# Performance work log

Hardware: AMD Instinct MI355X
Metric: run time of the kernel (lower is better)

## Reference

```python
import jax, jax.numpy as jnp
import numpy as np

GMAX = 1.0   # args.gmax
GMIN = 0.01  # args.gmin
EPS = 0.1    # args.e_train


def setup_inputs() -> dict:
    key = jax.random.key(0)
    k1, k2, k3, k4 = jax.random.split(key, 4)
    N, B, NIN, NOUT, E = 8, 32, 128, 128, 1024
    # analog signals live in [0, 1]
    a_previous = jax.random.uniform(k1, (N, B, NIN, E), dtype=jnp.float32)
    # conductance params (clamped to [-gmax, gmax] in forward)
    theta = jax.random.uniform(k2, (NIN + 2, NOUT), dtype=jnp.float32) * 2.0 - 1.0
    # per-replica multiplicative noise seed in [0, 1); forward maps to 1 +- eps
    noise = jax.random.uniform(k3, (N, NIN + 2, NOUT), dtype=jnp.float32)
    # printed-tanh activation params eta = [offset, scale, shift, slope]
    eta = jnp.array([0.0, 1.0, 0.0, 1.0], dtype=jnp.float32) + 0.1 * jax.random.normal(k4, (4,), dtype=jnp.float32)
    return {"a_previous": a_previous, "theta": theta, "noise": noise, "eta": eta}


def reference(a_previous, theta, noise, eta):
    sg = jax.lax.stop_gradient
    # theta property: clamp + gmin pruning with straight-through estimator
    t = jnp.clip(theta, -GMAX, GMAX)
    t = jnp.where(jnp.abs(t) < GMIN, 0.0, t)
    theta_eff = sg(t) + theta - sg(theta)
    # theta_noisy: replicate over N with multiplicative uniform noise in [1-eps, 1+eps]
    theta_noisy = theta_eff[None, :, :] * ((noise * 2.0 - 1.0) * EPS + 1.0)  # [N, M, O], M = n_in+2
    # W: abs-normalized conductances per output column group
    abs_tn = jnp.abs(theta_noisy)
    W = abs_tn / (jnp.sum(abs_tn, axis=1, keepdims=True) + 1e-10)
    # sign masks (constants w.r.t. grad: values fully overwritten in torch)
    pos = sg((theta_noisy >= 0.0).astype(theta_noisy.dtype))
    neg = 1.0 - pos
    # a: [N, B, n_in, E] -> [N, B, E, n_in]; append ones and zeros columns
    a_r = jnp.transpose(a_previous, (0, 1, 3, 2))
    ones = jnp.ones(a_r.shape[:3] + (1,), a_r.dtype)
    zeros = jnp.zeros_like(ones)
    a_ext = jnp.concatenate([a_r, ones, zeros], axis=3)  # [N, B, E, M]
    # INV: unipolar complement; zero the last (zeros) column after inversion
    a_neg = (1.0 - a_ext).at[..., -1].set(0.0)
    # split-sign MAC: z [N, B, E, n_out]
    z = (jnp.einsum('nbem,nmo->nbeo', a_ext, W * pos)
         + jnp.einsum('nbem,nmo->nbeo', a_neg, W * neg))
    # printed tanh activation
    act = eta[0] + eta[1] * jnp.tanh((z - eta[2]) * eta[3])
    # back to [N, B, n_out, E]
    return jnp.transpose(act, (0, 1, 3, 2))
```

## Files before the change

kernel.cpp:

```cpp
#include <hip/hip_runtime.h>
#include <hip/hip_bf16.h>
#include <stdint.h>

#define N_REP 8
#define BATCH 32
#define NIN   128
#define NOUT  128
#define EDIM  1024
#define MDIM  130
#define ETILE 64
#define NGRP  32
#define GSTR  260

typedef __attribute__((ext_vector_type(8))) short short8;
typedef __attribute__((ext_vector_type(4))) float f32x4;

__device__ __forceinline__ unsigned short f2bf(float f) {
    union { float f; uint32_t u; } v;
    v.f = f;
    uint32_t u = v.u;
    uint32_t r = u + 0x7fffu + ((u >> 16) & 1u);
    return (unsigned short)(r >> 16);
}

__device__ __forceinline__ uint32_t pk2bf(float lo, float hi) {
    __hip_bfloat162 h = __float22bfloat162_rn(make_float2(lo, hi));
    uint32_t d;
    __builtin_memcpy(&d, &h, 4);
    return d;
}

__device__ __forceinline__ void gload_lds16(float* lds, const float* g) {
    __builtin_amdgcn_global_load_lds(
        (const __attribute__((address_space(1))) void*)g,
        (__attribute__((address_space(3))) void*)lds, 16, 0, 0);
}

__global__ __launch_bounds__(64)
void prep_kernel(const float* __restrict__ theta,
                 const float* __restrict__ noise,
                 unsigned short* __restrict__ Sg,
                 float* __restrict__ biasg) {
    const int n = blockIdx.x >> 7;
    const int o = blockIdx.x & 127;
    const int lane = threadIdx.x;

    const float* nb = noise + (size_t)n * MDIM * NOUT + o;
    auto tn_at = [&](int m) -> float {
        float t = theta[m * NOUT + o];
        t = fminf(fmaxf(t, -1.f), 1.f);
        if (fabsf(t) < 0.01f) t = 0.f;
        return t * fmaf(nb[m * NOUT], 0.2f, 0.9f);
    };

    const float t0 = tn_at(lane);
    const float t1 = tn_at(lane + 64);
    const float t2 = (lane < 2) ? tn_at(128 + lane) : 0.f;

    float s = fabsf(t0) + fabsf(t1) + fabsf(t2);
#pragma unroll
    for (int d = 1; d < 64; d <<= 1) s += __shfl_xor(s, d, 64);
    const float inv = 1.f / (s + 1e-10f);

    const float w0 = fabsf(t0) * inv, w1 = fabsf(t1) * inv;
    unsigned short* srow = Sg + ((size_t)n * NOUT + o) * NIN;
    srow[lane]      = f2bf(t0 >= 0.f ? w0 : -w0);
    srow[lane + 64] = f2bf(t1 >= 0.f ? w1 : -w1);

    float b = (t0 < 0.f ? w0 : 0.f) + (t1 < 0.f ? w1 : 0.f);
    if (lane == 0 && t2 >= 0.f) b += fabsf(t2) * inv;
#pragma unroll
    for (int d = 1; d < 64; d <<= 1) b += __shfl_xor(b, d, 64);
    if (lane == 0) biasg[n * NOUT + o] = b;
}

__global__ __launch_bounds__(256, 4)
void gemm_kernel(const float* __restrict__ a,
                 const unsigned short* __restrict__ Sg,
                 const float* __restrict__ biasg,
                 const float* __restrict__ eta,
                 float* __restrict__ out) {
    __shared__ float Alds[NGRP * GSTR];
    const int bid  = blockIdx.x;
    const int et   = bid & 15;
    const int nb   = bid >> 4;
    const int n    = nb >> 5;
    const int tid  = threadIdx.x;
    const int lane = tid & 63;
    const int w    = tid >> 6;
    const int r    = lane & 15;
    const int q    = lane >> 4;

    {
        const float* gp = a + (size_t)nb * (NIN * EDIM)
                            + (size_t)(w * 32 + q) * EDIM + et * ETILE + (r << 2);
        float* lp = &Alds[(w * 8) * GSTR];
#pragma unroll
        for (int t = 0; t < 8; ++t)
            gload_lds16(lp + t * GSTR, gp + (size_t)(t * 4) * EDIM);
    }

    const int o_base = (w & 1) << 6;
    const int e_base = (w >> 1) << 5;

    const float e0 = eta[0], e1 = eta[1], e2 = eta[2], e3 = eta[3];
    float bl[4];
#pragma unroll
    for (int fo = 0; fo < 4; ++fo)
        bl[fo] = biasg[n * NOUT + o_base + (fo << 4) + r];

    const unsigned short* sbase = Sg + ((size_t)(n * NOUT) << 7) + (q << 3);
    short8 sf[4];
#pragma unroll
    for (int fo = 0; fo < 4; ++fo)
        sf[fo] = *(const short8*)(sbase + ((size_t)(o_base + (fo << 4) + r) << 7));

    f32x4 acc[4][2];
#pragma unroll
    for (int fo = 0; fo < 4; ++fo)
#pragma unroll
        for (int fe = 0; fe < 2; ++fe)
            acc[fo][fe] = (f32x4){0.f, 0.f, 0.f, 0.f};

    __syncthreads();

#pragma unroll
    for (int ks = 0; ks < 4; ++ks) {
        short8 sfn[4];
        if (ks < 3) {
#pragma unroll
            for (int fo = 0; fo < 4; ++fo)
                sfn[fo] = *(const short8*)(sbase + ((size_t)(o_base + (fo << 4) + r) << 7)
                                                 + ((ks + 1) << 5));
        }
        short8 af[2];
#pragma unroll
        for (int fe = 0; fe < 2; ++fe) {
            const float* base = &Alds[(ks * 8 + q * 2) * GSTR + e_base + (fe << 4) + r];
            uint32_t d[4];
#pragma unroll
            for (int t = 0; t < 4; ++t) {
                const int j0 = 2 * t, j1 = 2 * t + 1;
                const float f0 = base[(j0 >> 2) * GSTR + (j0 & 3) * 64];
                const float f1 = base[(j1 >> 2) * GSTR + (j1 & 3) * 64];
                d[t] = pk2bf(f0, f1);
            }
            __builtin_memcpy(&af[fe], d, 16);
        }
#pragma unroll
        for (int fo = 0; fo < 4; ++fo)
#pragma unroll
            for (int fe = 0; fe < 2; ++fe)
                acc[fo][fe] = __builtin_amdgcn_mfma_f32_16x16x32_bf16(
                    af[fe], sf[fo], acc[fo][fe], 0, 0, 0);
        if (ks < 3) {
#pragma unroll
            for (int fo = 0; fo < 4; ++fo)
                sf[fo] = sfn[fo];
        }
    }

    float* obase = out + (size_t)nb * (NOUT * EDIM) + et * ETILE;
#pragma unroll
    for (int fo = 0; fo < 4; ++fo) {
        float* orow = obase + (size_t)(o_base + (fo << 4) + r) * EDIM;
        const float bv = bl[fo];
#pragma unroll
        for (int fe = 0; fe < 2; ++fe) {
            f32x4 res;
#pragma unroll
            for (int i = 0; i < 4; ++i) {
                const float z = acc[fo][fe][i] + bv;
                const float y = (z - e2) * e3;
                const float ex = __expf(2.f * y);
                const float th = 1.f - 2.f * __builtin_amdgcn_rcpf(ex + 1.f);
                res[i] = fmaf(e1, th, e0);
            }
            *(f32x4*)(orow + e_base + (fe << 4) + (q << 2)) = res;
        }
    }
}

extern "C" void kernel_launch(void* const* d_in, const int* in_sizes, int n_in,
                              void* d_out, int out_size, void* d_ws, size_t ws_size,
                              hipStream_t stream) {
    const float* a     = (const float*)d_in[0];
    const float* theta = (const float*)d_in[1];
    const float* noise = (const float*)d_in[2];
    const float* eta   = (const float*)d_in[3];
    float* out = (float*)d_out;

    unsigned short* Sg = (unsigned short*)d_ws;
    float* biasg = (float*)((char*)d_ws + (size_t)N_REP * NOUT * NIN * sizeof(unsigned short));

    prep_kernel<<<N_REP * NOUT, 64, 0, stream>>>(theta, noise, Sg, biasg);
    gemm_kernel<<<N_REP * BATCH * (EDIM / ETILE), 256, 0, stream>>>(a, Sg, biasg, eta, out);
}
```

Baseline: 261.0 us.

## Process four E-tiles per block with double-buffered LDS prefetch

```diff
diff --git a/kernel.cpp b/kernel.cpp
--- a/kernel.cpp
+++ b/kernel.cpp
@@ -9,6 +9,7 @@
 #define EDIM  1024
 #define MDIM  130
 #define ETILE 64
+#define NT    4
 #define NGRP  32
 #define GSTR  260
 
@@ -74,109 +75,121 @@
     if (lane == 0) biasg[n * NOUT + o] = b;
 }
 
-__global__ __launch_bounds__(256, 4)
+__global__ __launch_bounds__(256, 2)
 void gemm_kernel(const float* __restrict__ a,
                  const unsigned short* __restrict__ Sg,
                  const float* __restrict__ biasg,
                  const float* __restrict__ eta,
                  float* __restrict__ out) {
-    __shared__ float Alds[NGRP * GSTR];
+    __shared__ float Alds[2][NGRP * GSTR];
     const int bid  = blockIdx.x;
-    const int et   = bid & 15;
-    const int nb   = bid >> 4;
+    const int nb   = bid >> 2;
     const int n    = nb >> 5;
+    const int et0  = (bid & 3) << 2;
     const int tid  = threadIdx.x;
     const int lane = tid & 63;
     const int w    = tid >> 6;
     const int r    = lane & 15;
     const int q    = lane >> 4;
 
-    {
-        const float* gp = a + (size_t)nb * (NIN * EDIM)
-                            + (size_t)(w * 32 + q) * EDIM + et * ETILE + (r << 2);
-        float* lp = &Alds[(w * 8) * GSTR];
-#pragma unroll
-        for (int t = 0; t < 8; ++t)
-            gload_lds16(lp + t * GSTR, gp + (size_t)(t * 4) * EDIM);
-    }
+    const float* gbase = a + (size_t)nb * (NIN * EDIM)
+                           + (size_t)(w * 32 + q) * EDIM + et0 * ETILE + (r << 2);
+
+    auto stage = [&](int buf, int t) {
+        const float* gp = gbase + t * ETILE;
+        float* lp = &Alds[buf][(w * 8) * GSTR];
+#pragma unroll
+        for (int k = 0; k < 8; ++k)
+            gload_lds16(lp + k * GSTR, gp + (size_t)(k * 4) * EDIM);
+    };
+
+    stage(0, 0);
 
     const int o_base = (w & 1) << 6;
     const int e_base = (w >> 1) << 5;
 
-    const float e0 = eta[0], e1 = eta[1], e2 = eta[2], e3 = eta[3];
+    float e0 = eta[0], e1 = eta[1], e2 = eta[2], e3 = eta[3];
+    asm volatile("" : "+v"(e0), "+v"(e1), "+v"(e2), "+v"(e3));
     float bl[4];
 #pragma unroll
     for (int fo = 0; fo < 4; ++fo)
         bl[fo] = biasg[n * NOUT + o_base + (fo << 4) + r];
 
     const unsigned short* sbase = Sg + ((size_t)(n * NOUT) << 7) + (q << 3);
-    short8 sf[4];
-#pragma unroll
-    for (int fo = 0; fo < 4; ++fo)
-        sf[fo] = *(const short8*)(sbase + ((size_t)(o_base + (fo << 4) + r) << 7));
-
-    f32x4 acc[4][2];
-#pragma unroll
-    for (int fo = 0; fo < 4; ++fo)
-#pragma unroll
-        for (int fe = 0; fe < 2; ++fe)
-            acc[fo][fe] = (f32x4){0.f, 0.f, 0.f, 0.f};
+    short8 sfr[4][4];
+#pragma unroll
+    for (int ks = 0; ks < 4; ++ks)
+#pragma unroll
+        for (int fo = 0; fo < 4; ++fo)
+            sfr[ks][fo] = *(const short8*)(sbase + ((size_t)(o_base + (fo << 4) + r) << 7)
+                                                 + (ks << 5));
 
     __syncthreads();
 
-#pragma unroll
-    for (int ks = 0; ks < 4; ++ks) {
-        short8 sfn[4];
-        if (ks < 3) {
+    float* obase0 = out + (size_t)nb * (NOUT * EDIM) + et0 * ETILE;
+
+#pragma unroll
+    for (int t = 0; t < NT; ++t) {
+        const int cur = t & 1;
+        if (t + 1 < NT) stage(cur ^ 1, t + 1);
+        __builtin_amdgcn_sched_barrier(0);
+
+        f32x4 acc[4][2];
+#pragma unroll
+        for (int fo = 0; fo < 4; ++fo)
+#pragma unroll
+            for (int fe = 0; fe < 2; ++fe)
+                acc[fo][fe] = (f32x4){0.f, 0.f, 0.f, 0.f};
+
+#pragma unroll
+        for (int ks = 0; ks < 4; ++ks) {
+            short8 af[2];
+#pragma unroll
+            for (int fe = 0; fe < 2; ++fe) {
+                const float* base = &Alds[cur][(ks * 8 + q * 2) * GSTR + e_base + (fe << 4) + r];
+                uint32_t d[4];
+#pragma unroll
+                for (int tt = 0; tt < 4; ++tt) {
+                    const int j0 = 2 * tt, j1 = 2 * tt + 1;
+                    const float f0 = base[(j0 >> 2) * GSTR + (j0 & 3) * 64];
+                    const float f1 = base[(j1 >> 2) * GSTR + (j1 & 3) * 64];
+                    d[tt] = pk2bf(f0, f1);
+                }
+                __builtin_memcpy(&af[fe], d, 16);
+            }
 #pragma unroll
             for (int fo = 0; fo < 4; ++fo)
-                sfn[fo] = *(const short8*)(sbase + ((size_t)(o_base + (fo << 4) + r) << 7)
-                                                 + ((ks + 1) << 5));
+#pragma unroll
+                for (int fe = 0; fe < 2; ++fe)
+                    acc[fo][fe] = __builtin_amdgcn_mfma_f32_16x16x32_bf16(
+                        af[fe], sfr[ks][fo], acc[fo][fe], 0, 0, 0);
         }
-        short8 af[2];
-#pragma unroll
-        for (int fe = 0; fe < 2; ++fe) {
-            const float* base = &Alds[(ks * 8 + q * 2) * GSTR + e_base + (fe << 4) + r];
-            uint32_t d[4];
-#pragma unroll
-            for (int t = 0; t < 4; ++t) {
-                const int j0 = 2 * t, j1 = 2 * t + 1;
-                const float f0 = base[(j0 >> 2) * GSTR + (j0 & 3) * 64];
-                const float f1 = base[(j1 >> 2) * GSTR + (j1 & 3) * 64];
-                d[t] = pk2bf(f0, f1);
+
+        float* obase = obase0 + t * ETILE;
+#pragma unroll
+        for (int fo = 0; fo < 4; ++fo) {
+            float* orow = obase + (size_t)(o_base + (fo << 4) + r) * EDIM;
+            const float bv = bl[fo];
+#pragma unroll
+            for (int fe = 0; fe < 2; ++fe) {
+                f32x4 res;
+#pragma unroll
+                for (int i = 0; i < 4; ++i) {
+                    const float z = acc[fo][fe][i] + bv;
+                    const float y = (z - e2) * e3;
+                    const float ex = __expf(2.f * y);
+                    const float th = 1.f - 2.f * __builtin_amdgcn_rcpf(ex + 1.f);
+                    res[i] = fmaf(e1, th, e0);
+                }
+                *(f32x4*)(orow + e_base + (fe << 4) + (q << 2)) = res;
             }
-            __builtin_memcpy(&af[fe], d, 16);
         }
-#pragma unroll
-        for (int fo = 0; fo < 4; ++fo)
-#pragma unroll
-            for (int fe = 0; fe < 2; ++fe)
-                acc[fo][fe] = __builtin_amdgcn_mfma_f32_16x16x32_bf16(
-                    af[fe], sf[fo], acc[fo][fe], 0, 0, 0);
-        if (ks < 3) {
-#pragma unroll
-            for (int fo = 0; fo < 4; ++fo)
-                sf[fo] = sfn[fo];
-        }
-    }
-
-    float* obase = out + (size_t)nb * (NOUT * EDIM) + et * ETILE;
-#pragma unroll
-    for (int fo = 0; fo < 4; ++fo) {
-        float* orow = obase + (size_t)(o_base + (fo << 4) + r) * EDIM;
-        const float bv = bl[fo];
-#pragma unroll
-        for (int fe = 0; fe < 2; ++fe) {
-            f32x4 res;
-#pragma unroll
-            for (int i = 0; i < 4; ++i) {
-                const float z = acc[fo][fe][i] + bv;
-                const float y = (z - e2) * e3;
-                const float ex = __expf(2.f * y);
-                const float th = 1.f - 2.f * __builtin_amdgcn_rcpf(ex + 1.f);
-                res[i] = fmaf(e1, th, e0);
-            }
-            *(f32x4*)(orow + e_base + (fe << 4) + (q << 2)) = res;
+
+        if (t + 1 < NT) {
+            __builtin_amdgcn_sched_barrier(0);
+            asm volatile("s_waitcnt vmcnt(8)" ::: "memory");
+            __builtin_amdgcn_s_barrier();
+            __builtin_amdgcn_sched_barrier(0);
         }
     }
 }
@@ -194,5 +207,5 @@
     float* biasg = (float*)((char*)d_ws + (size_t)N_REP * NOUT * NIN * sizeof(unsigned short));
 
     prep_kernel<<<N_REP * NOUT, 64, 0, stream>>>(theta, noise, Sg, biasg);
-    gemm_kernel<<<N_REP * BATCH * (EDIM / ETILE), 256, 0, stream>>>(a, Sg, biasg, eta, out);
-}
+    gemm_kernel<<<N_REP * BATCH * (EDIM / ETILE / NT), 256, 0, stream>>>(a, Sg, biasg, eta, out);
+}
```

Result: faster. 254.0 us (-2.7%).

## Convert A to packed bf16 in registers before LDS, use 128-thread blocks

Applied to the files above, without the earlier changes.

```diff
diff --git a/kernel.cpp b/kernel.cpp
--- a/kernel.cpp
+++ b/kernel.cpp
@@ -9,8 +9,7 @@
 #define EDIM  1024
 #define MDIM  130
 #define ETILE 64
-#define NGRP  32
-#define GSTR  260
+#define SE    68
 
 typedef __attribute__((ext_vector_type(8))) short short8;
 typedef __attribute__((ext_vector_type(4))) float f32x4;
@@ -28,12 +27,6 @@
     uint32_t d;
     __builtin_memcpy(&d, &h, 4);
     return d;
-}
-
-__device__ __forceinline__ void gload_lds16(float* lds, const float* g) {
-    __builtin_amdgcn_global_load_lds(
-        (const __attribute__((address_space(1))) void*)g,
-        (__attribute__((address_space(3))) void*)lds, 16, 0, 0);
 }
 
 __global__ __launch_bounds__(64)
@@ -74,13 +67,13 @@
     if (lane == 0) biasg[n * NOUT + o] = b;
 }
 
-__global__ __launch_bounds__(256, 4)
+__global__ __launch_bounds__(128, 4)
 void gemm_kernel(const float* __restrict__ a,
                  const unsigned short* __restrict__ Sg,
                  const float* __restrict__ biasg,
                  const float* __restrict__ eta,
                  float* __restrict__ out) {
-    __shared__ float Alds[NGRP * GSTR];
+    __shared__ uint32_t Alds[64 * SE];
     const int bid  = blockIdx.x;
     const int et   = bid & 15;
     const int nb   = bid >> 4;
@@ -92,72 +85,69 @@
     const int q    = lane >> 4;
 
     {
-        const float* gp = a + (size_t)nb * (NIN * EDIM)
-                            + (size_t)(w * 32 + q) * EDIM + et * ETILE + (r << 2);
-        float* lp = &Alds[(w * 8) * GSTR];
+        const float* abase = a + (size_t)nb * (NIN * EDIM) + et * ETILE;
+        const int e4  = (tid & 15) << 2;
+        const int mp0 = tid >> 4;
+        float4 va[8], vb[8];
 #pragma unroll
-        for (int t = 0; t < 8; ++t)
-            gload_lds16(lp + t * GSTR, gp + (size_t)(t * 4) * EDIM);
+        for (int it = 0; it < 8; ++it) {
+            const int mp = mp0 + (it << 3);
+            va[it] = *(const float4*)(abase + (size_t)(2 * mp) * EDIM + e4);
+            vb[it] = *(const float4*)(abase + (size_t)(2 * mp + 1) * EDIM + e4);
+        }
+#pragma unroll
+        for (int it = 0; it < 8; ++it) {
+            const int mp = mp0 + (it << 3);
+            uint4 d;
+            d.x = pk2bf(va[it].x, vb[it].x);
+            d.y = pk2bf(va[it].y, vb[it].y);
+            d.z = pk2bf(va[it].z, vb[it].z);
+            d.w = pk2bf(va[it].w, vb[it].w);
+            *(uint4*)&Alds[mp * SE + e4] = d;
+        }
     }
+    __syncthreads();
 
-    const int o_base = (w & 1) << 6;
-    const int e_base = (w >> 1) << 5;
+    const int o_base = w << 6;
 
-    const float e0 = eta[0], e1 = eta[1], e2 = eta[2], e3 = eta[3];
+    float e0 = eta[0], e1 = eta[1], e2 = eta[2], e3 = eta[3];
+    asm volatile("" : "+v"(e0), "+v"(e1), "+v"(e2), "+v"(e3));
     float bl[4];
 #pragma unroll
     for (int fo = 0; fo < 4; ++fo)
         bl[fo] = biasg[n * NOUT + o_base + (fo << 4) + r];
 
-    const unsigned short* sbase = Sg + ((size_t)(n * NOUT) << 7) + (q << 3);
-    short8 sf[4];
-#pragma unroll
-    for (int fo = 0; fo < 4; ++fo)
-        sf[fo] = *(const short8*)(sbase + ((size_t)(o_base + (fo << 4) + r) << 7));
-
-    f32x4 acc[4][2];
+    f32x4 acc[4][4];
 #pragma unroll
     for (int fo = 0; fo < 4; ++fo)
 #pragma unroll
-        for (int fe = 0; fe < 2; ++fe)
+        for (int fe = 0; fe < 4; ++fe)
             acc[fo][fe] = (f32x4){0.f, 0.f, 0.f, 0.f};
 
-    __syncthreads();
-
+    const unsigned short* sbase = Sg + ((size_t)(n * NOUT) << 7) + (q << 3);
 #pragma unroll
     for (int ks = 0; ks < 4; ++ks) {
-        short8 sfn[4];
-        if (ks < 3) {
+        short8 sf[4];
 #pragma unroll
-            for (int fo = 0; fo < 4; ++fo)
-                sfn[fo] = *(const short8*)(sbase + ((size_t)(o_base + (fo << 4) + r) << 7)
-                                                 + ((ks + 1) << 5));
-        }
-        short8 af[2];
+        for (int fo = 0; fo < 4; ++fo)
+            sf[fo] = *(const short8*)(sbase + ((size_t)(o_base + (fo << 4) + r) << 7)
+                                             + (ks << 5));
+        const int mpb = (ks << 4) + (q << 2);
+        short8 af[4];
 #pragma unroll
-        for (int fe = 0; fe < 2; ++fe) {
-            const float* base = &Alds[(ks * 8 + q * 2) * GSTR + e_base + (fe << 4) + r];
+        for (int fe = 0; fe < 4; ++fe) {
             uint32_t d[4];
 #pragma unroll
-            for (int t = 0; t < 4; ++t) {
-                const int j0 = 2 * t, j1 = 2 * t + 1;
-                const float f0 = base[(j0 >> 2) * GSTR + (j0 & 3) * 64];
-                const float f1 = base[(j1 >> 2) * GSTR + (j1 & 3) * 64];
-                d[t] = pk2bf(f0, f1);
-            }
+            for (int jj = 0; jj < 4; ++jj)
+                d[jj] = Alds[(mpb + jj) * SE + (fe << 4) + r];
             __builtin_memcpy(&af[fe], d, 16);
         }
 #pragma unroll
         for (int fo = 0; fo < 4; ++fo)
 #pragma unroll
-            for (int fe = 0; fe < 2; ++fe)
+            for (int fe = 0; fe < 4; ++fe)
                 acc[fo][fe] = __builtin_amdgcn_mfma_f32_16x16x32_bf16(
                     af[fe], sf[fo], acc[fo][fe], 0, 0, 0);
-        if (ks < 3) {
-#pragma unroll
-            for (int fo = 0; fo < 4; ++fo)
-                sf[fo] = sfn[fo];
-        }
     }
 
     float* obase = out + (size_t)nb * (NOUT * EDIM) + et * ETILE;
@@ -166,7 +156,7 @@
         float* orow = obase + (size_t)(o_base + (fo << 4) + r) * EDIM;
         const float bv = bl[fo];
 #pragma unroll
-        for (int fe = 0; fe < 2; ++fe) {
+        for (int fe = 0; fe < 4; ++fe) {
             f32x4 res;
 #pragma unroll
             for (int i = 0; i < 4; ++i) {
@@ -176,7 +166,7 @@
                 const float th = 1.f - 2.f * __builtin_amdgcn_rcpf(ex + 1.f);
                 res[i] = fmaf(e1, th, e0);
             }
-            *(f32x4*)(orow + e_base + (fe << 4) + (q << 2)) = res;
+            *(f32x4*)(orow + (fe << 4) + (q << 2)) = res;
         }
     }
 }
@@ -194,5 +184,5 @@
     float* biasg = (float*)((char*)d_ws + (size_t)N_REP * NOUT * NIN * sizeof(unsigned short));
 
     prep_kernel<<<N_REP * NOUT, 64, 0, stream>>>(theta, noise, Sg, biasg);
-    gemm_kernel<<<N_REP * BATCH * (EDIM / ETILE), 256, 0, stream>>>(a, Sg, biasg, eta, out);
+    gemm_kernel<<<N_REP * BATCH * (EDIM / ETILE), 128, 0, stream>>>(a, Sg, biasg, eta, out);
 }
```

Measured after the change: 258.2 us. No clear change (-1.1%).
